# Kernel tuning notes

Measured on AMD Instinct MI355X. Metric: run time of the kernel, lower is better.

## Reference

```python
import jax, jax.numpy as jnp
import numpy as np

B, T, N, D, F, ORDER = 16, 12, 1024, 64, 64, 2
EPS = 1e-5  # BatchNorm eps (eval mode, running stats)


def setup_inputs() -> dict:
    key = jax.random.key(0)
    ks = jax.random.split(key, 8)
    C_eff = (ORDER + 1) * D  # (order*support_len + 1) * c_in = 192
    return {
        "x": jax.random.normal(ks[0], (B, T, N, D), jnp.float32),
        "A": jax.random.uniform(ks[1], (B, N, N), jnp.float32),  # dynamic per-sample adjacency
        "conv_w": jax.random.normal(ks[2], (F, C_eff), jnp.float32) / np.float32(np.sqrt(C_eff)),
        "conv_b": jnp.zeros((F,), jnp.float32),
        "bn_gamma": jnp.ones((F,), jnp.float32),
        "bn_beta": jnp.zeros((F,), jnp.float32),
        "bn_mean": 0.1 * jax.random.normal(ks[3], (F,), jnp.float32),
        "bn_var": jax.random.uniform(ks[4], (F,), jnp.float32) + 0.5,
        "gru_ff_w": jax.random.normal(ks[5], (T, 2 * F, 2 * F), jnp.float32) / np.float32(np.sqrt(2 * F)),
        "gru_ff_b": jnp.zeros((T, 2 * F), jnp.float32),
        "gru_zff_w": jax.random.normal(ks[6], (T, 2 * F, F), jnp.float32) / np.float32(np.sqrt(2 * F)),
        "gru_zff_b": jnp.zeros((T, F), jnp.float32),
    }


def _forward(x, A, conv_w, conv_b, bn_gamma, bn_beta, bn_mean, bn_var,
             gru_ff_w, gru_ff_b, gru_zff_w, gru_zff_b):
    # ---- DiffusionGraphEncoder ----
    xt = jnp.transpose(x, (0, 3, 2, 1))  # (B, C, N, T), matches torch transpose(1,3)
    outs = [xt]
    cur = xt
    for _ in range(ORDER):  # nconv: einsum('ncvl,nwv->ncwl')
        cur = jnp.einsum('bcvt,bwv->bcwt', cur, A)
        outs.append(cur)
    h = jnp.concatenate(outs, axis=1)        # (B, 3C, N, T)
    h = jnp.transpose(h, (0, 3, 2, 1))       # (B, T, N, C_eff)
    # ---- MLP1x1: 1x1 conv + eval-mode BatchNorm + relu ----
    y = jnp.einsum('btnc,fc->btnf', h, conv_w) + conv_b
    y = (y - bn_mean) * jax.lax.rsqrt(bn_var + EPS) * bn_gamma + bn_beta
    y = jax.nn.relu(y)  # dropout is identity at inference
    # ---- GRUEncoder: distinct GRUCellLite per timestep ----
    xs = jnp.transpose(y, (1, 0, 2, 3))      # (T, B, N, F)
    h0 = jnp.zeros((B, N, F), y.dtype)

    def step(hprev, inp):
        xt_, wff, bff, wzff, bzff = inp
        ru = jax.nn.sigmoid(jnp.concatenate([xt_, hprev], -1) @ wff + bff)
        r, u = ru[..., :F], ru[..., F:]
        z = jnp.tanh(jnp.concatenate([xt_, r * hprev], -1) @ wzff + bzff)
        hn = u * z + (1.0 - u) * hprev
        return hn, hn

    _, hs = jax.lax.scan(step, h0, (xs, gru_ff_w, gru_ff_b, gru_zff_w, gru_zff_b))
    return jnp.transpose(hs, (1, 0, 2, 3))   # (B, T, N, F)


def reference(x, A, conv_w, conv_b, bn_gamma, bn_beta, bn_mean, bn_var,
              gru_ff_w, gru_ff_b, gru_zff_w, gru_zff_b):
    return _forward(x, A, conv_w, conv_b, bn_gamma, bn_beta, bn_mean, bn_var,
                    gru_ff_w, gru_ff_b, gru_zff_w, gru_zff_b)
```

## Files before the change

### kernel.cpp

```cpp
#include <hip/hip_runtime.h>
#include <cstdint>
#include <cstddef>

#define NB 16
#define TT 12
#define NN 1024
#define DD 64
#define FF 64
#define JT 768

typedef __attribute__((ext_vector_type(8))) short v8s;
typedef __attribute__((ext_vector_type(4))) short v4s;
typedef __attribute__((ext_vector_type(4))) float v4f;

__device__ __forceinline__ float sigmoidf_(float v) { return 1.0f / (1.0f + expf(-v)); }
__device__ __forceinline__ float fsig(float v) {
    return __fdividef(1.0f, 1.0f + __expf(-v));
}
__device__ __forceinline__ float ftanh(float v) {
    v = fminf(fmaxf(v, -15.0f), 15.0f);
    const float e = __expf(2.0f * v);
    return __fdividef(e - 1.0f, e + 1.0f);
}

__device__ __forceinline__ float bf2f(unsigned short h) {
    union { unsigned int u; float f; } x; x.u = ((unsigned int)h) << 16; return x.f;
}
__device__ __forceinline__ unsigned short f2bf(float f) {
    union { float f; unsigned int u; } x; x.f = f;
    return (unsigned short)((x.u + 0x7fffu + ((x.u >> 16) & 1u)) >> 16);
}

__device__ __forceinline__ void gload16(const void* g, void* lds) {
    __builtin_amdgcn_global_load_lds(
        (const __attribute__((address_space(1))) void*)g,
        (__attribute__((address_space(3))) void*)lds, 16, 0, 0);
}

__global__ __launch_bounds__(256) void split_A(
    const float* __restrict__ A, unsigned short* __restrict__ Ah,
    unsigned short* __restrict__ Al)
{
    const size_t i0 = ((size_t)blockIdx.x * 256 + threadIdx.x) * 16;
    float v[16];
#pragma unroll
    for (int s = 0; s < 4; ++s)
        *(float4*)&v[s * 4] = *(const float4*)&A[i0 + s * 4];
    v8s h0, h1, l0, l1;
#pragma unroll
    for (int q = 0; q < 8; ++q) {
        unsigned short h = f2bf(v[q]);
        h0[q] = (short)h; l0[q] = (short)f2bf(v[q] - bf2f(h));
    }
#pragma unroll
    for (int q = 0; q < 8; ++q) {
        unsigned short h = f2bf(v[8 + q]);
        h1[q] = (short)h; l1[q] = (short)f2bf(v[8 + q] - bf2f(h));
    }
    *(v8s*)&Ah[i0] = h0; *(v8s*)&Ah[i0 + 8] = h1;
    *(v8s*)&Al[i0] = l0; *(v8s*)&Al[i0 + 8] = l1;
}

__global__ __launch_bounds__(256) void xsplitT(
    const float* __restrict__ x, unsigned short* __restrict__ Th,
    unsigned short* __restrict__ Tl)
{
    __shared__ float tile[64][68];
    const int v0 = blockIdx.x * 64, t = blockIdx.y, b = blockIdx.z;
    const int tid = threadIdx.x;
    {
        const int r = tid >> 2, q = (tid & 3) * 16;
#pragma unroll
        for (int s = 0; s < 4; ++s) {
            const float4 w = *(const float4*)&x[(((size_t)b * TT + t) * NN + v0 + r) * DD + q + s * 4];
            tile[r][q + s * 4 + 0] = w.x; tile[r][q + s * 4 + 1] = w.y;
            tile[r][q + s * 4 + 2] = w.z; tile[r][q + s * 4 + 3] = w.w;
        }
    }
    __syncthreads();
    {
        const int d = tid >> 2, vc = (tid & 3) * 16;
        const size_t base = ((size_t)b * JT + t * 64 + d) * 1024 + v0 + vc;
        v8s h0, h1, l0, l1;
#pragma unroll
        for (int s = 0; s < 8; ++s) {
            const float f = tile[vc + s][d];
            unsigned short h = f2bf(f);
            h0[s] = (short)h; l0[s] = (short)f2bf(f - bf2f(h));
        }
#pragma unroll
        for (int s = 0; s < 8; ++s) {
            const float f = tile[vc + 8 + s][d];
            unsigned short h = f2bf(f);
            h1[s] = (short)h; l1[s] = (short)f2bf(f - bf2f(h));
        }
        *(v8s*)&Th[base] = h0; *(v8s*)&Th[base + 8] = h1;
        *(v8s*)&Tl[base] = l0; *(v8s*)&Tl[base + 8] = l1;
    }
}

template<bool PAIROUT>
__global__ __launch_bounds__(256, 2) void gemm_bf(
    const unsigned short* __restrict__ Ah, const unsigned short* __restrict__ Al,
    const unsigned short* __restrict__ Bh, const unsigned short* __restrict__ Bl,
    unsigned short* __restrict__ Ch, unsigned short* __restrict__ Cl,
    float* __restrict__ Cf)
{
    __shared__ unsigned short LA[2][2][4096];
    __shared__ unsigned short LB[2][2][6144];

    const int wg = blockIdx.x;
    const int nlin = (wg & 7) * 64 + (wg >> 3);
    const int b  = nlin >> 5;
    const int rr = nlin & 31;
    const int m0 = (rr >> 2) * 128, n0 = (rr & 3) * 192;

    const int tid = threadIdx.x, lane = tid & 63, wid = tid >> 6;
    const int lr = lane & 15, hi = lane >> 4;
    const int wr = wid >> 1, wc = wid & 1;

    auto stage = [&](int buf, int kt) {
        const int rA = lane >> 2, kc = (lane & 3) * 8;
#pragma unroll
        for (int p = 0; p < 2; ++p) {
            const int c = wid * 2 + p;
            const size_t ga = ((size_t)b * 1024 + m0 + c * 16 + rA) * 1024 + kt * 32 + kc;
            gload16(Ah + ga, &LA[buf][0][c * 512]);
            gload16(Al + ga, &LA[buf][1][c * 512]);
        }
#pragma unroll
        for (int p = 0; p < 3; ++p) {
            const int c = wid * 3 + p;
            const size_t gb = ((size_t)b * JT + n0 + c * 16 + rA) * 1024 + kt * 32 + kc;
            gload16(Bh + gb, &LB[buf][0][c * 512]);
            gload16(Bl + gb, &LB[buf][1][c * 512]);
        }
    };

    v4f acc[4][6];
#pragma unroll
    for (int i = 0; i < 4; ++i)
#pragma unroll
        for (int j = 0; j < 6; ++j) acc[i][j] = (v4f){0.f, 0.f, 0.f, 0.f};

    stage(0, 0);
    __syncthreads();
    int cur = 0;
    for (int kt = 0; kt < 32; ++kt) {
        if (kt + 1 < 32) stage(cur ^ 1, kt + 1);
        v8s ah[4], al[4], bh[6], bl[6];
#pragma unroll
        for (int f = 0; f < 4; ++f) {
            const int m = wr * 64 + f * 16 + lr;
            ah[f] = *(const v8s*)&LA[cur][0][m * 32 + hi * 8];
            al[f] = *(const v8s*)&LA[cur][1][m * 32 + hi * 8];
        }
#pragma unroll
        for (int f = 0; f < 6; ++f) {
            const int n = wc * 96 + f * 16 + lr;
            bh[f] = *(const v8s*)&LB[cur][0][n * 32 + hi * 8];
            bl[f] = *(const v8s*)&LB[cur][1][n * 32 + hi * 8];
        }
#pragma unroll
        for (int fi = 0; fi < 4; ++fi)
#pragma unroll
            for (int fj = 0; fj < 6; ++fj) {
                acc[fi][fj] = __builtin_amdgcn_mfma_f32_16x16x32_bf16(ah[fi], bh[fj], acc[fi][fj], 0, 0, 0);
                acc[fi][fj] = __builtin_amdgcn_mfma_f32_16x16x32_bf16(ah[fi], bl[fj], acc[fi][fj], 0, 0, 0);
                acc[fi][fj] = __builtin_amdgcn_mfma_f32_16x16x32_bf16(al[fi], bh[fj], acc[fi][fj], 0, 0, 0);
            }
        __syncthreads();
        cur ^= 1;
    }

#pragma unroll
    for (int fi = 0; fi < 4; ++fi)
#pragma unroll
        for (int fj = 0; fj < 6; ++fj) {
            const int n  = n0 + wc * 96 + fj * 16 + lr;
            const int mb = m0 + wr * 64 + fi * 16 + hi * 4;
            const size_t o = ((size_t)b * JT + n) * 1024 + mb;
            if (PAIROUT) {
                v4s vh, vl;
#pragma unroll
                for (int r = 0; r < 4; ++r) {
                    const float v = acc[fi][fj][r];
                    const unsigned short h = f2bf(v);
                    vh[r] = (short)h; vl[r] = (short)f2bf(v - bf2f(h));
                }
                *(v4s*)&Ch[o] = vh;
                *(v4s*)&Cl[o] = vl;
            } else {
                float4 v = {acc[fi][fj][0], acc[fi][fj][1], acc[fi][fj][2], acc[fi][fj][3]};
                *(float4*)&Cf[o] = v;
            }
        }
}

template<bool XFROMX>
__global__ __launch_bounds__(256, 4) void gemm_f32(
    const float* __restrict__ Aop, const float* __restrict__ Xin,
    float* __restrict__ Xout)
{
    __shared__ float As[2][16 * 132];
    __shared__ float Bs[2][16 * 128];
    const int wg  = blockIdx.x;
    const int nlin = (wg & 7) * 96 + (wg >> 3);
    const int b  = nlin / 48;
    const int rr = nlin % 48;
    const int rb = rr / 6, cb = rr % 6;
    const int w0 = rb * 128, j0 = cb * 128;
    const int tid = threadIdx.x;
    const int rg = tid >> 4, cg = tid & 15;
    const int row0 = rg * 8;

    auto stage = [&](int buf, int kt) {
        const float* Ab = Aop + (size_t)b * NN * NN;
#pragma unroll
        for (int p = 0; p < 2; ++p) {
            const int c  = tid + p * 256;
            const int w  = c >> 2;
            const int k4 = (c & 3) * 4;
            const float4 v = *(const float4*)&Ab[(size_t)(w0 + w) * NN + kt * 16 + k4];
            As[buf][(k4 + 0) * 132 + w] = v.x;
            As[buf][(k4 + 1) * 132 + w] = v.y;
            As[buf][(k4 + 2) * 132 + w] = v.z;
            As[buf][(k4 + 3) * 132 + w] = v.w;
        }
#pragma unroll
        for (int p = 0; p < 2; ++p) {
            const int c = tid + p * 256;
            const int k = c >> 5;
            const int j = (c & 31) * 4;
            float4 v;
            if (XFROMX) {
                const int t = cb * 2 + (j >> 6);
                const int d = j & 63;
                v = *(const float4*)&Xin[(((size_t)b * TT + t) * NN + (size_t)kt * 16 + k) * DD + d];
            } else {
                v = *(const float4*)&Xin[((size_t)b * NN + (size_t)kt * 16 + k) * JT + j0 + j];
            }
            *(float4*)&Bs[buf][k * 128 + j] = v;
        }
    };

    float acc[8][8];
#pragma unroll
    for (int i = 0; i < 8; ++i)
#pragma unroll
        for (int j = 0; j < 8; ++j) acc[i][j] = 0.0f;

    stage(0, 0);
    __syncthreads();
    int cur = 0;
    for (int kt = 0; kt < 64; ++kt) {
        if (kt + 1 < 64) stage(cur ^ 1, kt + 1);
#pragma unroll
        for (int k = 0; k < 16; ++k) {
            float a[8], bb[8];
            *(float4*)&a[0]  = *(const float4*)&As[cur][k * 132 + row0];
            *(float4*)&a[4]  = *(const float4*)&As[cur][k * 132 + row0 + 4];
            *(float4*)&bb[0] = *(const float4*)&Bs[cur][k * 128 + cg * 4];
            *(float4*)&bb[4] = *(const float4*)&Bs[cur][k * 128 + 64 + cg * 4];
#pragma unroll
            for (int i = 0; i < 8; ++i)
#pragma unroll
                for (int j = 0; j < 8; ++j)
                    acc[i][j] = fmaf(a[i], bb[j], acc[i][j]);
        }
        __syncthreads();
        cur ^= 1;
    }
#pragma unroll
    for (int i = 0; i < 8; ++i) {
        float4 v0 = {acc[i][0], acc[i][1], acc[i][2], acc[i][3]};
        float4 v1 = {acc[i][4], acc[i][5], acc[i][6], acc[i][7]};
        float* dst = Xout + ((size_t)b * NN + w0 + row0 + i) * JT + j0;
        *(float4*)&dst[cg * 4]      = v0;
        *(float4*)&dst[64 + cg * 4] = v1;
    }
}

template<bool PAIRS>
__global__ __launch_bounds__(256) void conv_bn_relu(
    const float* __restrict__ x,
    const unsigned short* __restrict__ X1h, const unsigned short* __restrict__ X1l,
    const float* __restrict__ X2T,
    const float* __restrict__ X1f, const float* __restrict__ X2f,
    const float* __restrict__ W,
    const float* __restrict__ convb, const float* __restrict__ gamma,
    const float* __restrict__ beta,  const float* __restrict__ mean,
    const float* __restrict__ var,   float* __restrict__ y)
{
    __shared__ float As[64][132];
    __shared__ float Ws[64][68];
    const int nb = blockIdx.x, t = blockIdx.y, b = blockIdx.z;
    const int n0 = nb * 128;
    const int tid = threadIdx.x;
    const int rg = tid >> 4, cg = tid & 15;
    const int row0 = rg * 8, f0 = cg * 4;

    float acc[8][4];
#pragma unroll
    for (int i = 0; i < 8; ++i)
#pragma unroll
        for (int j = 0; j < 4; ++j) acc[i][j] = 0.0f;

    for (int kt = 0; kt < 3; ++kt) {
        __syncthreads();
        if (kt == 0) {
            const float* src = x + (((size_t)b * TT + t) * NN + n0) * DD;
#pragma unroll
            for (int p = 0; p < 8; ++p) {
                const int row = (tid >> 4) + p * 16;
                const int c4  = (tid & 15) * 4;
                const float4 v = *(const float4*)&src[(size_t)row * DD + c4];
                As[c4 + 0][row] = v.x; As[c4 + 1][row] = v.y;
                As[c4 + 2][row] = v.z; As[c4 + 3][row] = v.w;
            }
        } else if (PAIRS) {
            if (kt == 1) {
#pragma unroll
                for (int p = 0; p < 4; ++p) {
                    const int pos = p * 256 + tid;
                    const int c = pos >> 4, rw = (pos & 15) * 8;
                    const size_t o = ((size_t)b * JT + t * 64 + c) * 1024 + n0 + rw;
                    const v8s hv = *(const v8s*)&X1h[o];
                    const v8s lv = *(const v8s*)&X1l[o];
#pragma unroll
                    for (int q = 0; q < 8; ++q)
                        As[c][rw + q] = bf2f((unsigned short)hv[q]) + bf2f((unsigned short)lv[q]);
                }
            } else {
#pragma unroll
                for (int p = 0; p < 8; ++p) {
                    const int pos = p * 256 + tid;
                    const int c = pos >> 5, rw = (pos & 31) * 4;
                    const float4 v = *(const float4*)&X2T[((size_t)b * JT + t * 64 + c) * 1024 + n0 + rw];
                    As[c][rw + 0] = v.x; As[c][rw + 1] = v.y;
                    As[c][rw + 2] = v.z; As[c][rw + 3] = v.w;
                }
            }
        } else {
            const float* src = ((kt == 1) ? X1f : X2f) + ((size_t)b * NN + n0) * JT + t * DD;
#pragma unroll
            for (int p = 0; p < 8; ++p) {
                const int row = (tid >> 4) + p * 16;
                const int c4  = (tid & 15) * 4;
                const float4 v = *(const float4*)&src[(size_t)row * JT + c4];
                As[c4 + 0][row] = v.x; As[c4 + 1][row] = v.y;
                As[c4 + 2][row] = v.z; As[c4 + 3][row] = v.w;
            }
        }
#pragma unroll
        for (int p = 0; p < 4; ++p) {
            const int f  = (tid >> 4) + p * 16;
            const int c4 = (tid & 15) * 4;
            const float4 v = *(const float4*)&W[f * 192 + kt * 64 + c4];
            Ws[c4 + 0][f] = v.x; Ws[c4 + 1][f] = v.y;
            Ws[c4 + 2][f] = v.z; Ws[c4 + 3][f] = v.w;
        }
        __syncthreads();
#pragma unroll
        for (int k = 0; k < 64; ++k) {
            float a[8], w[4];
            *(float4*)&a[0] = *(const float4*)&As[k][row0];
            *(float4*)&a[4] = *(const float4*)&As[k][row0 + 4];
            *(float4*)&w[0] = *(const float4*)&Ws[k][f0];
#pragma unroll
            for (int i = 0; i < 8; ++i)
#pragma unroll
                for (int j = 0; j < 4; ++j)
                    acc[i][j] = fmaf(a[i], w[j], acc[i][j]);
        }
    }
    float s[4], off[4];
#pragma unroll
    for (int j = 0; j < 4; ++j) {
        const int f = f0 + j;
        const float sc = gamma[f] / sqrtf(var[f] + 1e-5f);
        s[j]   = sc;
        off[j] = (convb[f] - mean[f]) * sc + beta[f];
    }
#pragma unroll
    for (int i = 0; i < 8; ++i) {
        float4 v;
        v.x = fmaxf(acc[i][0] * s[0] + off[0], 0.0f);
        v.y = fmaxf(acc[i][1] * s[1] + off[1], 0.0f);
        v.z = fmaxf(acc[i][2] * s[2] + off[2], 0.0f);
        v.w = fmaxf(acc[i][3] * s[3] + off[3], 0.0f);
        *(float4*)&y[(((size_t)b * TT + t) * NN + n0 + row0 + i) * FF + f0] = v;
    }
}

__global__ __launch_bounds__(256) void wprep3(
    const float* __restrict__ wff, const float* __restrict__ wzff,
    unsigned short* __restrict__ WF, unsigned short* __restrict__ WZ)
{
    const int t = blockIdx.x;
    unsigned short* F = WF + (size_t)t * 40960;
    for (int e = threadIdx.x; e < 8192; e += 256) {
        const int o = e >> 6, k = e & 63;
        const float vx = wff[((size_t)t * 128 + k) * 128 + o];
        const unsigned short xh = f2bf(vx);
        const float r1 = vx - bf2f(xh);
        const unsigned short xm = f2bf(r1);
        const unsigned short xl = f2bf(r1 - bf2f(xm));
        F[0 * 8192 + o * 64 + k] = xh;
        F[1 * 8192 + o * 64 + k] = xm;
        F[2 * 8192 + o * 64 + k] = xl;
        const float vh = wff[((size_t)t * 128 + 64 + k) * 128 + o];
        const unsigned short hh = f2bf(vh);
        const unsigned short hl = f2bf(vh - bf2f(hh));
        F[3 * 8192 + o * 64 + k] = hh;
        F[4 * 8192 + o * 64 + k] = hl;
    }
    unsigned short* Z = WZ + (size_t)t * 20480;
    for (int e = threadIdx.x; e < 4096; e += 256) {
        const int o = e >> 6, k = e & 63;
        const float vx = wzff[((size_t)t * 128 + k) * 64 + o];
        const unsigned short xh = f2bf(vx);
        const float r1 = vx - bf2f(xh);
        const unsigned short xm = f2bf(r1);
        const unsigned short xl = f2bf(r1 - bf2f(xm));
        Z[0 * 4096 + o * 64 + k] = xh;
        Z[1 * 4096 + o * 64 + k] = xm;
        Z[2 * 4096 + o * 64 + k] = xl;
        const float vr = wzff[((size_t)t * 128 + 64 + k) * 64 + o];
        const unsigned short rh = f2bf(vr);
        const unsigned short rl = f2bf(vr - bf2f(rh));
        Z[3 * 4096 + o * 64 + k] = rh;
        Z[4 * 4096 + o * 64 + k] = rl;
    }
}

__global__ __launch_bounds__(256, 2) void gru7(
    const float* __restrict__ y,
    const unsigned short* __restrict__ WF, const unsigned short* __restrict__ WZ,
    const float* __restrict__ bff, const float* __restrict__ bzff,
    float* __restrict__ out)
{
    __shared__ unsigned short Ahp[4096];
    __shared__ unsigned short Rhp[4096];
    __shared__ float Hs[32][68];

    const int tid = threadIdx.x, lane = tid & 63, w = tid >> 6;
    const int lr = lane & 15, hi = lane >> 4;
    const int b = blockIdx.x >> 5, n0 = (blockIdx.x & 31) * 32;

    for (int i = tid; i < 4096; i += 256) { Ahp[i] = 0; Rhp[i] = 0; }
    for (int i = tid; i < 32 * 68; i += 256) (&Hs[0][0])[i] = 0.0f;
    __syncthreads();

    auto loadx = [&](int t, v8s xa[2][2][3]) {
        const float* yb = y + (((size_t)b * TT + t) * NN + n0) * 64;
#pragma unroll
        for (int mf = 0; mf < 2; ++mf)
#pragma unroll
            for (int kc = 0; kc < 2; ++kc) {
                const int m = mf * 16 + lr;
                float xv[8];
                *(float4*)&xv[0] = *(const float4*)&yb[m * 64 + kc * 32 + hi * 8];
                *(float4*)&xv[4] = *(const float4*)&yb[m * 64 + kc * 32 + hi * 8 + 4];
                v8s h3, m3, l3;
#pragma unroll
                for (int q = 0; q < 8; ++q) {
                    const float v = xv[q];
                    const unsigned short hh = f2bf(v);
                    const float r1 = v - bf2f(hh);
                    const unsigned short mm = f2bf(r1);
                    const unsigned short ll = f2bf(r1 - bf2f(mm));
                    h3[q] = (short)hh; m3[q] = (short)mm; l3[q] = (short)ll;
                }
                xa[mf][kc][0] = h3; xa[mf][kc][1] = m3; xa[mf][kc][2] = l3;
            }
    };
    auto xru_mfma = [&](int t, const v8s xa[2][2][3], v4f xacc[2][2]) {
#pragma unroll
        for (int of = 0; of < 2; ++of) {
            const int o = (2 * w + of) * 16 + lr;
            v8s wx[2][3];
#pragma unroll
            for (int kc = 0; kc < 2; ++kc)
#pragma unroll
                for (int lev = 0; lev < 3; ++lev)
                    wx[kc][lev] = *(const v8s*)&WF[((size_t)t * 5 + lev) * 8192 + o * 64 + kc * 32 + hi * 8];
#pragma unroll
            for (int mf = 0; mf < 2; ++mf)
#pragma unroll
                for (int kc = 0; kc < 2; ++kc) {
                    v4f a = xacc[of][mf];
                    a = __builtin_amdgcn_mfma_f32_16x16x32_bf16(xa[mf][kc][0], wx[kc][0], a, 0, 0, 0);
                    a = __builtin_amdgcn_mfma_f32_16x16x32_bf16(xa[mf][kc][0], wx[kc][1], a, 0, 0, 0);
                    a = __builtin_amdgcn_mfma_f32_16x16x32_bf16(xa[mf][kc][1], wx[kc][0], a, 0, 0, 0);
                    a = __builtin_amdgcn_mfma_f32_16x16x32_bf16(xa[mf][kc][0], wx[kc][2], a, 0, 0, 0);
                    a = __builtin_amdgcn_mfma_f32_16x16x32_bf16(xa[mf][kc][1], wx[kc][1], a, 0, 0, 0);
                    a = __builtin_amdgcn_mfma_f32_16x16x32_bf16(xa[mf][kc][2], wx[kc][0], a, 0, 0, 0);
                    xacc[of][mf] = a;
                }
        }
    };
    auto xz_mfma = [&](int t, const v8s xa[2][2][3], v4f xacc[2][2]) {
#pragma unroll
        for (int of = 0; of < 2; ++of) {
            const int o = (w & 1) * 32 + of * 16 + lr;
            v8s wx[2][3];
#pragma unroll
            for (int kc = 0; kc < 2; ++kc)
#pragma unroll
                for (int lev = 0; lev < 3; ++lev)
                    wx[kc][lev] = *(const v8s*)&WZ[((size_t)t * 5 + lev) * 4096 + o * 64 + kc * 32 + hi * 8];
#pragma unroll
            for (int mf = 0; mf < 2; ++mf)
#pragma unroll
                for (int kc = 0; kc < 2; ++kc) {
                    v4f a = xacc[of][mf];
                    a = __builtin_amdgcn_mfma_f32_16x16x32_bf16(xa[mf][kc][0], wx[kc][0], a, 0, 0, 0);
                    a = __builtin_amdgcn_mfma_f32_16x16x32_bf16(xa[mf][kc][0], wx[kc][1], a, 0, 0, 0);
                    a = __builtin_amdgcn_mfma_f32_16x16x32_bf16(xa[mf][kc][1], wx[kc][0], a, 0, 0, 0);
                    a = __builtin_amdgcn_mfma_f32_16x16x32_bf16(xa[mf][kc][0], wx[kc][2], a, 0, 0, 0);
                    a = __builtin_amdgcn_mfma_f32_16x16x32_bf16(xa[mf][kc][1], wx[kc][1], a, 0, 0, 0);
                    a = __builtin_amdgcn_mfma_f32_16x16x32_bf16(xa[mf][kc][2], wx[kc][0], a, 0, 0, 0);
                    xacc[of][mf] = a;
                }
        }
    };

    v4f xru[2][2], xz[2][2];
#pragma unroll
    for (int of = 0; of < 2; ++of)
#pragma unroll
        for (int mf = 0; mf < 2; ++mf) {
            xru[of][mf] = (v4f){0.f, 0.f, 0.f, 0.f};
            xz[of][mf]  = (v4f){0.f, 0.f, 0.f, 0.f};
        }
    {
        v8s xa0[2][2][3];
        loadx(0, xa0);
        xru_mfma(0, xa0, xru);
        xz_mfma(0, xa0, xz);
    }

    for (int t = 0; t < TT; ++t) {
        const int hasNext = (t + 1 < TT);
        v8s ha[2][2][2];
#pragma unroll
        for (int mf = 0; mf < 2; ++mf)
#pragma unroll
            for (int kc = 0; kc < 2; ++kc) {
                const int m = mf * 16 + lr;
                const int base = m * 128 + kc * 32 + hi * 8;
                const int sw = (m & 7) << 3;
                ha[mf][kc][0] = *(const v8s*)&Ahp[base ^ sw];
                ha[mf][kc][1] = *(const v8s*)&Ahp[(base + 64) ^ sw];
            }

        v4f acc[2][2];
#pragma unroll
        for (int of = 0; of < 2; ++of)
#pragma unroll
            for (int mf = 0; mf < 2; ++mf) acc[of][mf] = xru[of][mf];

        v8s xan[2][2][3];
        v4f xruN[2][2], xzN[2][2];
#pragma unroll
        for (int of = 0; of < 2; ++of)
#pragma unroll
            for (int mf = 0; mf < 2; ++mf) {
                xruN[of][mf] = (v4f){0.f, 0.f, 0.f, 0.f};
                xzN[of][mf]  = (v4f){0.f, 0.f, 0.f, 0.f};
            }
        if (hasNext) loadx(t + 1, xan);

#pragma unroll
        for (int of = 0; of < 2; ++of) {
            const int o = (2 * w + of) * 16 + lr;
            v8s wh_[2][2];
#pragma unroll
            for (int kc = 0; kc < 2; ++kc)
#pragma unroll
                for (int lev = 0; lev < 2; ++lev)
                    wh_[kc][lev] = *(const v8s*)&WF[((size_t)t * 5 + 3 + lev) * 8192 + o * 64 + kc * 32 + hi * 8];
#pragma unroll
            for (int mf = 0; mf < 2; ++mf)
#pragma unroll
                for (int kc = 0; kc < 2; ++kc) {
                    v4f a = acc[of][mf];
                    a = __builtin_amdgcn_mfma_f32_16x16x32_bf16(ha[mf][kc][0], wh_[kc][0], a, 0, 0, 0);
                    a = __builtin_amdgcn_mfma_f32_16x16x32_bf16(ha[mf][kc][0], wh_[kc][1], a, 0, 0, 0);
                    a = __builtin_amdgcn_mfma_f32_16x16x32_bf16(ha[mf][kc][1], wh_[kc][0], a, 0, 0, 0);
                    acc[of][mf] = a;
                }
        }
        if (hasNext) xru_mfma(t + 1, xan, xruN);

        float u_[2][2][4];
#pragma unroll
        for (int of = 0; of < 2; ++of) {
            const int o = (2 * w + of) * 16 + lr;
            const float bv = bff[(size_t)t * 128 + o];
#pragma unroll
            for (int mf = 0; mf < 2; ++mf)
#pragma unroll
                for (int q = 0; q < 4; ++q) {
                    const float g = fsig(acc[of][mf][q] + bv);
                    if (w < 2) {
                        const int m = mf * 16 + hi * 4 + q;
                        const float rh = g * Hs[m][o];
                        const unsigned short h = f2bf(rh);
                        const unsigned short l = f2bf(rh - bf2f(h));
                        const int sw = (m & 7) << 3;
                        Rhp[(m * 128 + o) ^ sw]      = h;
                        Rhp[(m * 128 + 64 + o) ^ sw] = l;
                    } else {
                        u_[of][mf][q] = g;
                    }
                }
        }
        __syncthreads();

        v8s ra[2][2][2];
#pragma unroll
        for (int mf = 0; mf < 2; ++mf)
#pragma unroll
            for (int kc = 0; kc < 2; ++kc) {
                const int m = mf * 16 + lr;
                const int base = m * 128 + kc * 32 + hi * 8;
                const int sw = (m & 7) << 3;
                ra[mf][kc][0] = *(const v8s*)&Rhp[base ^ sw];
                ra[mf][kc][1] = *(const v8s*)&Rhp[(base + 64) ^ sw];
            }

        v4f accz[2][2];
#pragma unroll
        for (int of = 0; of < 2; ++of)
#pragma unroll
            for (int mf = 0; mf < 2; ++mf) accz[of][mf] = xz[of][mf];

#pragma unroll
        for (int of = 0; of < 2; ++of) {
            const int o = (w & 1) * 32 + of * 16 + lr;
            v8s wr_[2][2];
#pragma unroll
            for (int kc = 0; kc < 2; ++kc)
#pragma unroll
                for (int lev = 0; lev < 2; ++lev)
                    wr_[kc][lev] = *(const v8s*)&WZ[((size_t)t * 5 + 3 + lev) * 4096 + o * 64 + kc * 32 + hi * 8];
#pragma unroll
            for (int mf = 0; mf < 2; ++mf)
#pragma unroll
                for (int kc = 0; kc < 2; ++kc) {
                    v4f a = accz[of][mf];
                    a = __builtin_amdgcn_mfma_f32_16x16x32_bf16(ra[mf][kc][0], wr_[kc][0], a, 0, 0, 0);
                    a = __builtin_amdgcn_mfma_f32_16x16x32_bf16(ra[mf][kc][0], wr_[kc][1], a, 0, 0, 0);
                    a = __builtin_amdgcn_mfma_f32_16x16x32_bf16(ra[mf][kc][1], wr_[kc][0], a, 0, 0, 0);
                    accz[of][mf] = a;
                }
        }
        if (hasNext) xz_mfma(t + 1, xan, xzN);

        if (w >= 2) {
#pragma unroll
            for (int of = 0; of < 2; ++of) {
                const int o = (w & 1) * 32 + of * 16 + lr;
                const float bz = bzff[(size_t)t * 64 + o];
#pragma unroll
                for (int mf = 0; mf < 2; ++mf)
#pragma unroll
                    for (int q = 0; q < 4; ++q) {
                        const int m = mf * 16 + hi * 4 + q;
                        const float z = ftanh(accz[of][mf][q] + bz);
                        const float u = u_[of][mf][q];
                        const float hn = u * z + (1.0f - u) * Hs[m][o];
                        Hs[m][o] = hn;
                        const unsigned short h = f2bf(hn);
                        const unsigned short l = f2bf(hn - bf2f(h));
                        const int sw = (m & 7) << 3;
                        Ahp[(m * 128 + o) ^ sw]      = h;
                        Ahp[(m * 128 + 64 + o) ^ sw] = l;
                        out[(((size_t)b * TT + t) * NN + n0 + m) * 64 + o] = hn;
                    }
            }
        }
        __syncthreads();

#pragma unroll
        for (int of = 0; of < 2; ++of)
#pragma unroll
            for (int mf = 0; mf < 2; ++mf) {
                xru[of][mf] = xruN[of][mf];
                xz[of][mf]  = xzN[of][mf];
            }
    }
}

__global__ __launch_bounds__(256) void gru_all(
    const float* __restrict__ y,    const float* __restrict__ wff,
    const float* __restrict__ bff,  const float* __restrict__ wzff,
    const float* __restrict__ bzff, float* __restrict__ out)
{
    __shared__ float Xs[64][36];
    __shared__ float Hs[64][36];
    __shared__ float Rs[64][36];
    __shared__ float Us[64][36];
    __shared__ float Ws[64][132];
    const int tid = threadIdx.x;
    const int mb  = blockIdx.x;
    const int b = mb >> 5, n0 = (mb & 31) * 32;
    const int rg = tid >> 5;
    const int og = tid & 31;

    for (int i = tid; i < 64 * 36; i += 256) (&Hs[0][0])[i] = 0.0f;

    for (int t = 0; t < TT; ++t) {
        {
            const float* xt = y + (((size_t)b * TT + t) * NN + n0) * DD;
            const int m = tid >> 3, c0 = (tid & 7) * 8;
            const float4 v0 = *(const float4*)&xt[m * DD + c0];
            const float4 v1 = *(const float4*)&xt[m * DD + c0 + 4];
            Xs[c0 + 0][m] = v0.x; Xs[c0 + 1][m] = v0.y;
            Xs[c0 + 2][m] = v0.z; Xs[c0 + 3][m] = v0.w;
            Xs[c0 + 4][m] = v1.x; Xs[c0 + 5][m] = v1.y;
            Xs[c0 + 6][m] = v1.z; Xs[c0 + 7][m] = v1.w;
        }
        float acc[4][4];
#pragma unroll
        for (int i = 0; i < 4; ++i)
#pragma unroll
            for (int j = 0; j < 4; ++j) acc[i][j] = 0.0f;

#pragma unroll
        for (int half = 0; half < 2; ++half) {
            __syncthreads();
#pragma unroll
            for (int p = 0; p < 8; ++p) {
                const int kk = (tid >> 5) + p * 8;
                const int o4 = (tid & 31) * 4;
                *(float4*)&Ws[kk][o4] =
                    *(const float4*)&wff[((size_t)t * 128 + half * 64 + kk) * 128 + o4];
            }
            __syncthreads();
            const float (*Asrc)[36] = half ? Hs : Xs;
#pragma unroll 4
            for (int kk = 0; kk < 64; ++kk) {
                const float4 av = *(const float4*)&Asrc[kk][rg * 4];
                const float4 wv = *(const float4*)&Ws[kk][og * 4];
                const float a0 = av.x, a1 = av.y, a2 = av.z, a3 = av.w;
                acc[0][0] = fmaf(a0, wv.x, acc[0][0]); acc[0][1] = fmaf(a0, wv.y, acc[0][1]);
                acc[0][2] = fmaf(a0, wv.z, acc[0][2]); acc[0][3] = fmaf(a0, wv.w, acc[0][3]);
                acc[1][0] = fmaf(a1, wv.x, acc[1][0]); acc[1][1] = fmaf(a1, wv.y, acc[1][1]);
                acc[1][2] = fmaf(a1, wv.z, acc[1][2]); acc[1][3] = fmaf(a1, wv.w, acc[1][3]);
                acc[2][0] = fmaf(a2, wv.x, acc[2][0]); acc[2][1] = fmaf(a2, wv.y, acc[2][1]);
                acc[2][2] = fmaf(a2, wv.z, acc[2][2]); acc[2][3] = fmaf(a2, wv.w, acc[2][3]);
                acc[3][0] = fmaf(a3, wv.x, acc[3][0]); acc[3][1] = fmaf(a3, wv.y, acc[3][1]);
                acc[3][2] = fmaf(a3, wv.z, acc[3][2]); acc[3][3] = fmaf(a3, wv.w, acc[3][3]);
            }
        }
        {
            const float4 bb4 = *(const float4*)&bff[(size_t)t * 128 + og * 4];
            float g[4][4];
#pragma unroll
            for (int i = 0; i < 4; ++i) {
                g[i][0] = sigmoidf_(acc[i][0] + bb4.x);
                g[i][1] = sigmoidf_(acc[i][1] + bb4.y);
                g[i][2] = sigmoidf_(acc[i][2] + bb4.z);
                g[i][3] = sigmoidf_(acc[i][3] + bb4.w);
            }
            if (og < 16) {
#pragma unroll
                for (int i = 0; i < 4; ++i)
#pragma unroll
                    for (int j = 0; j < 4; ++j) {
                        const int f = og * 4 + j, m = rg * 4 + i;
                        Rs[f][m] = g[i][j] * Hs[f][m];
                    }
            } else {
#pragma unroll
                for (int i = 0; i < 4; ++i)
#pragma unroll
                    for (int j = 0; j < 4; ++j)
                        Us[og * 4 + j - 64][rg * 4 + i] = g[i][j];
            }
        }
        float accz[4][2];
#pragma unroll
        for (int i = 0; i < 4; ++i) { accz[i][0] = 0.0f; accz[i][1] = 0.0f; }

#pragma unroll
        for (int half = 0; half < 2; ++half) {
            __syncthreads();
#pragma unroll
            for (int p = 0; p < 4; ++p) {
                const int kk = (tid >> 4) + p * 16;
                const int f4 = (tid & 15) * 4;
                *(float4*)&Ws[kk][f4] =
                    *(const float4*)&wzff[((size_t)t * 128 + half * 64 + kk) * 64 + f4];
            }
            __syncthreads();
            const float (*Asrc)[36] = half ? Rs : Xs;
#pragma unroll 4
            for (int kk = 0; kk < 64; ++kk) {
                const float4 av = *(const float4*)&Asrc[kk][rg * 4];
                const float2 wv = *(const float2*)&Ws[kk][og * 2];
                accz[0][0] = fmaf(av.x, wv.x, accz[0][0]); accz[0][1] = fmaf(av.x, wv.y, accz[0][1]);
                accz[1][0] = fmaf(av.y, wv.x, accz[1][0]); accz[1][1] = fmaf(av.y, wv.y, accz[1][1]);
                accz[2][0] = fmaf(av.z, wv.x, accz[2][0]); accz[2][1] = fmaf(av.z, wv.y, accz[2][1]);
                accz[3][0] = fmaf(av.w, wv.x, accz[3][0]); accz[3][1] = fmaf(av.w, wv.y, accz[3][1]);
            }
        }
        {
            const float2 bz = *(const float2*)&bzff[(size_t)t * 64 + og * 2];
            const int f0_ = og * 2;
#pragma unroll
            for (int i = 0; i < 4; ++i) {
                const int m = rg * 4 + i;
                const float z0 = tanhf(accz[i][0] + bz.x);
                const float z1 = tanhf(accz[i][1] + bz.y);
                const float u0 = Us[f0_][m],     u1 = Us[f0_ + 1][m];
                const float h0 = Hs[f0_][m],     h1 = Hs[f0_ + 1][m];
                const float hn0 = u0 * z0 + (1.0f - u0) * h0;
                const float hn1 = u1 * z1 + (1.0f - u1) * h1;
                Hs[f0_][m] = hn0; Hs[f0_ + 1][m] = hn1;
                *(float2*)&out[(((size_t)b * TT + t) * NN + n0 + m) * FF + f0_] =
                    make_float2(hn0, hn1);
            }
        }
        __syncthreads();
    }
}

extern "C" void kernel_launch(void* const* d_in, const int* in_sizes, int n_in,
                              void* d_out, int out_size, void* d_ws, size_t ws_size,
                              hipStream_t stream)
{
    const float* x        = (const float*)d_in[0];
    const float* A        = (const float*)d_in[1];
    const float* conv_w   = (const float*)d_in[2];
    const float* conv_b   = (const float*)d_in[3];
    const float* bn_gamma = (const float*)d_in[4];
    const float* bn_beta  = (const float*)d_in[5];
    const float* bn_mean  = (const float*)d_in[6];
    const float* bn_var   = (const float*)d_in[7];
    const float* gru_ff_w  = (const float*)d_in[8];
    const float* gru_ff_b  = (const float*)d_in[9];
    const float* gru_zff_w = (const float*)d_in[10];
    const float* gru_zff_b = (const float*)d_in[11];
    float* out = (float*)d_out;
    char* w = (char*)d_ws;

    const size_t szA_bf  = (size_t)NB * NN * NN * 2;
    const size_t szXT_bf = (size_t)NB * JT * NN * 2;
    const size_t needFast = 2 * szA_bf + 2 * szXT_bf + 2 * szXT_bf;

    dim3 gconv(8, TT, NB);

    if (ws_size >= needFast) {
        unsigned short* Ah2 = (unsigned short*)(w);
        unsigned short* Al2 = (unsigned short*)(w + szA_bf);
        unsigned short* X1h = (unsigned short*)(w + 2 * szA_bf);
        unsigned short* X1l = (unsigned short*)(w + 2 * szA_bf + szXT_bf);
        char* slot = w + 2 * szA_bf + 2 * szXT_bf;
        unsigned short* xh = (unsigned short*)slot;
        unsigned short* xl = (unsigned short*)(slot + szXT_bf);
        float* X2T = (float*)slot;
        float* yb = (float*)w;
        unsigned short* WF = (unsigned short*)(w + 50331648);
        unsigned short* WZ = (unsigned short*)(w + 50331648 + 983040);

        xsplitT<<<dim3(16, TT, NB), 256, 0, stream>>>(x, xh, xl);
        split_A<<<4096, 256, 0, stream>>>(A, Ah2, Al2);
        gemm_bf<true ><<<512, 256, 0, stream>>>(Ah2, Al2, xh,  xl,  X1h, X1l, nullptr);
        gemm_bf<false><<<512, 256, 0, stream>>>(Ah2, Al2, X1h, X1l, nullptr, nullptr, X2T);
        conv_bn_relu<true><<<gconv, 256, 0, stream>>>(x, X1h, X1l, X2T, nullptr, nullptr,
                                                      conv_w, conv_b, bn_gamma, bn_beta,
                                                      bn_mean, bn_var, yb);
        wprep3<<<TT, 256, 0, stream>>>(gru_ff_w, gru_zff_w, WF, WZ);
        gru7<<<512, 256, 0, stream>>>(yb, WF, WZ, gru_ff_b, gru_zff_b, out);
    } else {
        const size_t szX = (size_t)NB * NN * JT;
        float* X1 = (float*)w;
        float* X2 = X1 + szX;
        float* yb = X2 + szX;
        gemm_f32<true ><<<768, 256, 0, stream>>>(A, x,  X1);
        gemm_f32<false><<<768, 256, 0, stream>>>(A, X1, X2);
        conv_bn_relu<false><<<gconv, 256, 0, stream>>>(x, nullptr, nullptr, nullptr, X1, X2,
                                                       conv_w, conv_b, bn_gamma, bn_beta,
                                                       bn_mean, bn_var, yb);
        gru_all<<<512, 256, 0, stream>>>(yb, gru_ff_w, gru_ff_b,
                                         gru_zff_w, gru_zff_b, out);
    }
}
```

Baseline: 446.8 us.

## Split GRU output tiles across 8 waves per block instead of 4

Result: slower. 637.4 us (+42.7%).

```diff
diff --git a/kernel.cpp b/kernel.cpp
--- a/kernel.cpp
+++ b/kernel.cpp
@@ -434,7 +434,7 @@
     }
 }
 
-__global__ __launch_bounds__(256, 2) void gru7(
+__global__ __launch_bounds__(512, 4) void gru10(
     const float* __restrict__ y,
     const unsigned short* __restrict__ WF, const unsigned short* __restrict__ WZ,
     const float* __restrict__ bff, const float* __restrict__ bzff,
@@ -448,8 +448,8 @@
     const int lr = lane & 15, hi = lane >> 4;
     const int b = blockIdx.x >> 5, n0 = (blockIdx.x & 31) * 32;
 
-    for (int i = tid; i < 4096; i += 256) { Ahp[i] = 0; Rhp[i] = 0; }
-    for (int i = tid; i < 32 * 68; i += 256) (&Hs[0][0])[i] = 0.0f;
+    for (int i = tid; i < 4096; i += 512) { Ahp[i] = 0; Rhp[i] = 0; }
+    for (int i = tid; i < 32 * 68; i += 512) (&Hs[0][0])[i] = 0.0f;
     __syncthreads();
 
     auto loadx = [&](int t, v8s xa[2][2][3]) {
@@ -475,65 +475,57 @@
                 xa[mf][kc][0] = h3; xa[mf][kc][1] = m3; xa[mf][kc][2] = l3;
             }
     };
-    auto xru_mfma = [&](int t, const v8s xa[2][2][3], v4f xacc[2][2]) {
-#pragma unroll
-        for (int of = 0; of < 2; ++of) {
-            const int o = (2 * w + of) * 16 + lr;
-            v8s wx[2][3];
-#pragma unroll
-            for (int kc = 0; kc < 2; ++kc)
-#pragma unroll
-                for (int lev = 0; lev < 3; ++lev)
-                    wx[kc][lev] = *(const v8s*)&WF[((size_t)t * 5 + lev) * 8192 + o * 64 + kc * 32 + hi * 8];
-#pragma unroll
-            for (int mf = 0; mf < 2; ++mf)
-#pragma unroll
-                for (int kc = 0; kc < 2; ++kc) {
-                    v4f a = xacc[of][mf];
-                    a = __builtin_amdgcn_mfma_f32_16x16x32_bf16(xa[mf][kc][0], wx[kc][0], a, 0, 0, 0);
-                    a = __builtin_amdgcn_mfma_f32_16x16x32_bf16(xa[mf][kc][0], wx[kc][1], a, 0, 0, 0);
-                    a = __builtin_amdgcn_mfma_f32_16x16x32_bf16(xa[mf][kc][1], wx[kc][0], a, 0, 0, 0);
-                    a = __builtin_amdgcn_mfma_f32_16x16x32_bf16(xa[mf][kc][0], wx[kc][2], a, 0, 0, 0);
-                    a = __builtin_amdgcn_mfma_f32_16x16x32_bf16(xa[mf][kc][1], wx[kc][1], a, 0, 0, 0);
-                    a = __builtin_amdgcn_mfma_f32_16x16x32_bf16(xa[mf][kc][2], wx[kc][0], a, 0, 0, 0);
-                    xacc[of][mf] = a;
-                }
-        }
+    auto xru_mfma = [&](int t, const v8s xa[2][2][3], v4f xacc[2]) {
+        const int o = w * 16 + lr;
+        v8s wx[2][3];
+#pragma unroll
+        for (int kc = 0; kc < 2; ++kc)
+#pragma unroll
+            for (int lev = 0; lev < 3; ++lev)
+                wx[kc][lev] = *(const v8s*)&WF[((size_t)t * 5 + lev) * 8192 + o * 64 + kc * 32 + hi * 8];
+#pragma unroll
+        for (int mf = 0; mf < 2; ++mf)
+#pragma unroll
+            for (int kc = 0; kc < 2; ++kc) {
+                v4f a = xacc[mf];
+                a = __builtin_amdgcn_mfma_f32_16x16x32_bf16(xa[mf][kc][0], wx[kc][0], a, 0, 0, 0);
+                a = __builtin_amdgcn_mfma_f32_16x16x32_bf16(xa[mf][kc][0], wx[kc][1], a, 0, 0, 0);
+                a = __builtin_amdgcn_mfma_f32_16x16x32_bf16(xa[mf][kc][1], wx[kc][0], a, 0, 0, 0);
+                a = __builtin_amdgcn_mfma_f32_16x16x32_bf16(xa[mf][kc][0], wx[kc][2], a, 0, 0, 0);
+                a = __builtin_amdgcn_mfma_f32_16x16x32_bf16(xa[mf][kc][1], wx[kc][1], a, 0, 0, 0);
+                a = __builtin_amdgcn_mfma_f32_16x16x32_bf16(xa[mf][kc][2], wx[kc][0], a, 0, 0, 0);
+                xacc[mf] = a;
+            }
     };
-    auto xz_mfma = [&](int t, const v8s xa[2][2][3], v4f xacc[2][2]) {
-#pragma unroll
-        for (int of = 0; of < 2; ++of) {
-            const int o = (w & 1) * 32 + of * 16 + lr;
-            v8s wx[2][3];
-#pragma unroll
-            for (int kc = 0; kc < 2; ++kc)
-#pragma unroll
-                for (int lev = 0; lev < 3; ++lev)
-                    wx[kc][lev] = *(const v8s*)&WZ[((size_t)t * 5 + lev) * 4096 + o * 64 + kc * 32 + hi * 8];
-#pragma unroll
-            for (int mf = 0; mf < 2; ++mf)
-#pragma unroll
-                for (int kc = 0; kc < 2; ++kc) {
-                    v4f a = xacc[of][mf];
-                    a = __builtin_amdgcn_mfma_f32_16x16x32_bf16(xa[mf][kc][0], wx[kc][0], a, 0, 0, 0);
-                    a = __builtin_amdgcn_mfma_f32_16x16x32_bf16(xa[mf][kc][0], wx[kc][1], a, 0, 0, 0);
-                    a = __builtin_amdgcn_mfma_f32_16x16x32_bf16(xa[mf][kc][1], wx[kc][0], a, 0, 0, 0);
-                    a = __builtin_amdgcn_mfma_f32_16x16x32_bf16(xa[mf][kc][0], wx[kc][2], a, 0, 0, 0);
-                    a = __builtin_amdgcn_mfma_f32_16x16x32_bf16(xa[mf][kc][1], wx[kc][1], a, 0, 0, 0);
-                    a = __builtin_amdgcn_mfma_f32_16x16x32_bf16(xa[mf][kc][2], wx[kc][0], a, 0, 0, 0);
-                    xacc[of][mf] = a;
-                }
-        }
+    auto xz_mfma = [&](int t, const v8s xa[2][2][3], v4f xacc[2]) {
+        const int o = (w & 3) * 16 + lr;
+        v8s wx[2][3];
+#pragma unroll
+        for (int kc = 0; kc < 2; ++kc)
+#pragma unroll
+            for (int lev = 0; lev < 3; ++lev)
+                wx[kc][lev] = *(const v8s*)&WZ[((size_t)t * 5 + lev) * 4096 + o * 64 + kc * 32 + hi * 8];
+#pragma unroll
+        for (int mf = 0; mf < 2; ++mf)
+#pragma unroll
+            for (int kc = 0; kc < 2; ++kc) {
+                v4f a = xacc[mf];
+                a = __builtin_amdgcn_mfma_f32_16x16x32_bf16(xa[mf][kc][0], wx[kc][0], a, 0, 0, 0);
+                a = __builtin_amdgcn_mfma_f32_16x16x32_bf16(xa[mf][kc][0], wx[kc][1], a, 0, 0, 0);
+                a = __builtin_amdgcn_mfma_f32_16x16x32_bf16(xa[mf][kc][1], wx[kc][0], a, 0, 0, 0);
+                a = __builtin_amdgcn_mfma_f32_16x16x32_bf16(xa[mf][kc][0], wx[kc][2], a, 0, 0, 0);
+                a = __builtin_amdgcn_mfma_f32_16x16x32_bf16(xa[mf][kc][1], wx[kc][1], a, 0, 0, 0);
+                a = __builtin_amdgcn_mfma_f32_16x16x32_bf16(xa[mf][kc][2], wx[kc][0], a, 0, 0, 0);
+                xacc[mf] = a;
+            }
     };
 
-    v4f xru[2][2], xz[2][2];
-#pragma unroll
-    for (int of = 0; of < 2; ++of)
-#pragma unroll
-        for (int mf = 0; mf < 2; ++mf) {
-            xru[of][mf] = (v4f){0.f, 0.f, 0.f, 0.f};
-            xz[of][mf]  = (v4f){0.f, 0.f, 0.f, 0.f};
-        }
+    v4f xru[2], xz[2];
+#pragma unroll
+    for (int mf = 0; mf < 2; ++mf) {
+        xru[mf] = (v4f){0.f, 0.f, 0.f, 0.f};
+        xz[mf]  = (v4f){0.f, 0.f, 0.f, 0.f};
+    }
     {
         v8s xa0[2][2][3];
         loadx(0, xa0);
@@ -555,26 +547,21 @@
                 ha[mf][kc][1] = *(const v8s*)&Ahp[(base + 64) ^ sw];
             }
 
-        v4f acc[2][2];
-#pragma unroll
-        for (int of = 0; of < 2; ++of)
-#pragma unroll
-            for (int mf = 0; mf < 2; ++mf) acc[of][mf] = xru[of][mf];
+        v4f acc[2];
+#pragma unroll
+        for (int mf = 0; mf < 2; ++mf) acc[mf] = xru[mf];
 
         v8s xan[2][2][3];
-        v4f xruN[2][2], xzN[2][2];
-#pragma unroll
-        for (int of = 0; of < 2; ++of)
-#pragma unroll
-            for (int mf = 0; mf < 2; ++mf) {
-                xruN[of][mf] = (v4f){0.f, 0.f, 0.f, 0.f};
-                xzN[of][mf]  = (v4f){0.f, 0.f, 0.f, 0.f};
-            }
+        v4f xruN[2], xzN[2];
+#pragma unroll
+        for (int mf = 0; mf < 2; ++mf) {
+            xruN[mf] = (v4f){0.f, 0.f, 0.f, 0.f};
+            xzN[mf]  = (v4f){0.f, 0.f, 0.f, 0.f};
+        }
         if (hasNext) loadx(t + 1, xan);
 
-#pragma unroll
-        for (int of = 0; of < 2; ++of) {
-            const int o = (2 * w + of) * 16 + lr;
+        {
+            const int o = w * 16 + lr;
             v8s wh_[2][2];
 #pragma unroll
             for (int kc = 0; kc < 2; ++kc)
@@ -585,26 +572,25 @@
             for (int mf = 0; mf < 2; ++mf)
 #pragma unroll
                 for (int kc = 0; kc < 2; ++kc) {
-                    v4f a = acc[of][mf];
+                    v4f a = acc[mf];
                     a = __builtin_amdgcn_mfma_f32_16x16x32_bf16(ha[mf][kc][0], wh_[kc][0], a, 0, 0, 0);
                     a = __builtin_amdgcn_mfma_f32_16x16x32_bf16(ha[mf][kc][0], wh_[kc][1], a, 0, 0, 0);
                     a = __builtin_amdgcn_mfma_f32_16x16x32_bf16(ha[mf][kc][1], wh_[kc][0], a, 0, 0, 0);
-                    acc[of][mf] = a;
+                    acc[mf] = a;
                 }
         }
         if (hasNext) xru_mfma(t + 1, xan, xruN);
 
-        float u_[2][2][4];
-#pragma unroll
-        for (int of = 0; of < 2; ++of) {
-            const int o = (2 * w + of) * 16 + lr;
+        float u_[2][4];
+        {
+            const int o = w * 16 + lr;
             const float bv = bff[(size_t)t * 128 + o];
 #pragma unroll
             for (int mf = 0; mf < 2; ++mf)
 #pragma unroll
                 for (int q = 0; q < 4; ++q) {
-                    const float g = fsig(acc[of][mf][q] + bv);
-                    if (w < 2) {
+                    const float g = fsig(acc[mf][q] + bv);
+                    if (w < 4) {
                         const int m = mf * 16 + hi * 4 + q;
                         const float rh = g * Hs[m][o];
                         const unsigned short h = f2bf(rh);
@@ -613,7 +599,7 @@
                         Rhp[(m * 128 + o) ^ sw]      = h;
                         Rhp[(m * 128 + 64 + o) ^ sw] = l;
                     } else {
-                        u_[of][mf][q] = g;
+                        u_[mf][q] = g;
                     }
                 }
         }
@@ -631,15 +617,12 @@
                 ra[mf][kc][1] = *(const v8s*)&Rhp[(base + 64) ^ sw];
             }
 
-        v4f accz[2][2];
-#pragma unroll
-        for (int of = 0; of < 2; ++of)
-#pragma unroll
-            for (int mf = 0; mf < 2; ++mf) accz[of][mf] = xz[of][mf];
-
-#pragma unroll
-        for (int of = 0; of < 2; ++of) {
-            const int o = (w & 1) * 32 + of * 16 + lr;
+        v4f accz[2];
+#pragma unroll
+        for (int mf = 0; mf < 2; ++mf) accz[mf] = xz[mf];
+
+        {
+            const int o = (w & 3) * 16 + lr;
             v8s wr_[2][2];
 #pragma unroll
             for (int kc = 0; kc < 2; ++kc)
@@ -650,47 +633,39 @@
             for (int mf = 0; mf < 2; ++mf)
 #pragma unroll
                 for (int kc = 0; kc < 2; ++kc) {
-                    v4f a = accz[of][mf];
+                    v4f a = accz[mf];
                     a = __builtin_amdgcn_mfma_f32_16x16x32_bf16(ra[mf][kc][0], wr_[kc][0], a, 0, 0, 0);
                     a = __builtin_amdgcn_mfma_f32_16x16x32_bf16(ra[mf][kc][0], wr_[kc][1], a, 0, 0, 0);
                     a = __builtin_amdgcn_mfma_f32_16x16x32_bf16(ra[mf][kc][1], wr_[kc][0], a, 0, 0, 0);
-                    accz[of][mf] = a;
+                    accz[mf] = a;
                 }
         }
         if (hasNext) xz_mfma(t + 1, xan, xzN);
 
-        if (w >= 2) {
-#pragma unroll
-            for (int of = 0; of < 2; ++of) {
-                const int o = (w & 1) * 32 + of * 16 + lr;
-                const float bz = bzff[(size_t)t * 64 + o];
-#pragma unroll
-                for (int mf = 0; mf < 2; ++mf)
-#pragma unroll
-                    for (int q = 0; q < 4; ++q) {
-                        const int m = mf * 16 + hi * 4 + q;
-                        const float z = ftanh(accz[of][mf][q] + bz);
-                        const float u = u_[of][mf][q];
-                        const float hn = u * z + (1.0f - u) * Hs[m][o];
-                        Hs[m][o] = hn;
-                        const unsigned short h = f2bf(hn);
-                        const unsigned short l = f2bf(hn - bf2f(h));
-                        const int sw = (m & 7) << 3;
-                        Ahp[(m * 128 + o) ^ sw]      = h;
-                        Ahp[(m * 128 + 64 + o) ^ sw] = l;
-                        out[(((size_t)b * TT + t) * NN + n0 + m) * 64 + o] = hn;
-                    }
-            }
+        if (w >= 4) {
+            const int o = (w & 3) * 16 + lr;
+            const float bz = bzff[(size_t)t * 64 + o];
+#pragma unroll
+            for (int mf = 0; mf < 2; ++mf)
+#pragma unroll
+                for (int q = 0; q < 4; ++q) {
+                    const int m = mf * 16 + hi * 4 + q;
+                    const float z = ftanh(accz[mf][q] + bz);
+                    const float u = u_[mf][q];
+                    const float hn = u * z + (1.0f - u) * Hs[m][o];
+                    Hs[m][o] = hn;
+                    const unsigned short h = f2bf(hn);
+                    const unsigned short l = f2bf(hn - bf2f(h));
+                    const int sw = (m & 7) << 3;
+                    Ahp[(m * 128 + o) ^ sw]      = h;
+                    Ahp[(m * 128 + 64 + o) ^ sw] = l;
+                    out[(((size_t)b * TT + t) * NN + n0 + m) * 64 + o] = hn;
+                }
         }
         __syncthreads();
 
 #pragma unroll
-        for (int of = 0; of < 2; ++of)
-#pragma unroll
-            for (int mf = 0; mf < 2; ++mf) {
-                xru[of][mf] = xruN[of][mf];
-                xz[of][mf]  = xzN[of][mf];
-            }
+        for (int mf = 0; mf < 2; ++mf) { xru[mf] = xruN[mf]; xz[mf] = xzN[mf]; }
     }
 }
 
@@ -875,7 +850,7 @@
                                                       conv_w, conv_b, bn_gamma, bn_beta,
                                                       bn_mean, bn_var, yb);
         wprep3<<<TT, 256, 0, stream>>>(gru_ff_w, gru_zff_w, WF, WZ);
-        gru7<<<512, 256, 0, stream>>>(yb, WF, WZ, gru_ff_b, gru_zff_b, out);
+        gru10<<<512, 512, 0, stream>>>(yb, WF, WZ, gru_ff_b, gru_zff_b, out);
     } else {
         const size_t szX = (size_t)NB * NN * JT;
         float* X1 = (float*)w;
```
